# Kernel optimization log

Measured on AMD Instinct MI355X. Metric: run time of the kernel, lower is better.

Reference implementation:

```python
import jax, jax.numpy as jnp
import numpy as np

NEG_SLOPE = 0.2

def _glorot(key, shape):
    fan_in, fan_out = shape[0], shape[1]
    lim = (6.0 / (fan_in + fan_out)) ** 0.5
    return jax.random.uniform(key, shape, jnp.float32, -lim, lim)

def setup_inputs() -> dict:
    key = jax.random.key(0)
    N, E = 50000, 1000000
    node_dim, edge_dim, hidden = 64, 16, 32
    H1 = 4
    ks = jax.random.split(key, 20)
    x = jax.random.normal(ks[0], (N, node_dim), jnp.float32)
    edge_index = jax.random.randint(ks[1], (2, E), 0, N, jnp.int64)
    edge_attr = jax.random.normal(ks[2], (E, edge_dim), jnp.float32)
    d = dict(x=x, edge_index=edge_index, edge_attr=edge_attr)
    # gat1: GATv2Conv(node_dim -> hidden, heads=4, edge_dim)
    d['W1l'] = _glorot(ks[3], (node_dim, H1 * hidden)); d['b1l'] = jnp.zeros((H1 * hidden,), jnp.float32)
    d['W1r'] = _glorot(ks[4], (node_dim, H1 * hidden)); d['b1r'] = jnp.zeros((H1 * hidden,), jnp.float32)
    d['W1e'] = _glorot(ks[5], (edge_dim, H1 * hidden))
    d['att1'] = _glorot(ks[6], (H1, hidden))
    d['bias1'] = jnp.zeros((H1 * hidden,), jnp.float32)
    # gat2: GATv2Conv(4*hidden -> hidden, heads=1, edge_dim)
    d['W2l'] = _glorot(ks[7], (H1 * hidden, hidden)); d['b2l'] = jnp.zeros((hidden,), jnp.float32)
    d['W2r'] = _glorot(ks[8], (H1 * hidden, hidden)); d['b2r'] = jnp.zeros((hidden,), jnp.float32)
    d['W2e'] = _glorot(ks[9], (edge_dim, hidden))
    d['att2'] = _glorot(ks[10], (1, hidden))
    d['bias2'] = jnp.zeros((hidden,), jnp.float32)
    # edge classifier: Linear(2*hidden+edge_dim -> hidden), ReLU, Linear(hidden -> 1)
    ein = 2 * hidden + edge_dim
    d['Wc1'] = _glorot(ks[11], (ein, hidden)); d['bc1'] = jnp.zeros((hidden,), jnp.float32)
    d['Wc2'] = _glorot(ks[12], (hidden, 1)); d['bc2'] = jnp.zeros((1,), jnp.float32)
    return d

def _gatv2(x, src, dst, eattr, Wl, bl, Wr, br, We, att, bias, H, C):
    # src/dst already include self loops; eattr matches.
    N = x.shape[0]
    xl = (x @ Wl + bl).reshape(N, H, C)   # source transform
    xr = (x @ Wr + br).reshape(N, H, C)   # target transform
    ea = (eattr @ We).reshape(-1, H, C)
    m = jax.nn.leaky_relu(xl[src] + xr[dst] + ea, NEG_SLOPE)   # [E,H,C]
    alpha = jnp.einsum('ehc,hc->eh', m, att)                   # [E,H]
    amax = jax.ops.segment_max(alpha, dst, num_segments=N)
    ealpha = jnp.exp(alpha - amax[dst])
    denom = jax.ops.segment_sum(ealpha, dst, num_segments=N)
    alpha = ealpha / denom[dst]
    out = jax.ops.segment_sum(xl[src] * alpha[..., None], dst, num_segments=N)
    return out.reshape(N, H * C) + bias

def reference(x, edge_index, edge_attr, W1l, b1l, W1r, b1r, W1e, att1, bias1,
              W2l, b2l, W2r, b2r, W2e, att2, bias2, Wc1, bc1, Wc2, bc2):
    N = x.shape[0]
    src, dst = edge_index[0], edge_index[1]
    # add self loops with edge_attr fill_value='mean' (per-target mean of incoming edge attrs)
    loop_attr = jax.ops.segment_sum(edge_attr, dst, num_segments=N)
    deg = jax.ops.segment_sum(jnp.ones((dst.shape[0],), edge_attr.dtype), dst, num_segments=N)
    loop_attr = loop_attr / jnp.maximum(deg, 1.0)[:, None]
    ar = jnp.arange(N, dtype=src.dtype)
    src2 = jnp.concatenate([src, ar]); dst2 = jnp.concatenate([dst, ar])
    eattr2 = jnp.concatenate([edge_attr, loop_attr], axis=0)
    h = _gatv2(x, src2, dst2, eattr2, W1l, b1l, W1r, b1r, W1e, att1, bias1, 4, 32)
    h = jax.nn.elu(h)
    h = _gatv2(h, src2, dst2, eattr2, W2l, b2l, W2r, b2r, W2e, att2, bias2, 1, 32)
    h = jax.nn.elu(h)
    edge_emb = jnp.concatenate([h[src], h[dst]], axis=1)         # [E, 2*hidden]
    feats = jnp.concatenate([edge_emb, edge_attr], axis=1)       # [E, 2*hidden+edge_dim]
    hid = jax.nn.relu(feats @ Wc1 + bc1)
    logits = (hid @ Wc2 + bc2).squeeze(-1)                        # [E]
    return logits
```

## Files before the change

kernel.cpp:

```cpp
#include <hip/hip_runtime.h>

namespace {

constexpr int NN  = 50000;
constexpr int EE  = 1000000;
constexpr int EE2 = EE + NN;
constexpr int ND  = 64;
constexpr int F1  = 128;
constexpr int F2  = 32;
constexpr float NEG = 0.2f;

typedef unsigned short ushort_t;
typedef _Float16 half_t;
typedef _Float16 half2_t __attribute__((ext_vector_type(2)));

__device__ __forceinline__ unsigned short f2h(float f) {
  union { half_t h; unsigned short u; } c; c.h = (half_t)f; return c.u;
}
__device__ __forceinline__ float h2f(unsigned short v) {
  union { unsigned short u; half_t h; } c; c.u = v; return (float)c.h;
}
__device__ __forceinline__ half2_t u2h2(unsigned u) {
  union { unsigned u; half2_t h; } c; c.u = u; return c.h;
}
__device__ __forceinline__ unsigned pack2(float x, float y) {
  return (unsigned)f2h(x) | ((unsigned)f2h(y) << 16);
}
__device__ __forceinline__ half2_t mkh2(float x, float y) {
  half2_t r; r.x = (half_t)x; r.y = (half_t)y; return r;
}

#if __has_builtin(__builtin_amdgcn_fdot2)
#define FDOT2(a, b, c) __builtin_amdgcn_fdot2((a), (b), (c), false)
#else
#define FDOT2(a, b, c) ((float)(a).x * (float)(b).x + (float)(a).y * (float)(b).y + (c))
#endif

__global__ __launch_bounds__(256) void k_deg(const int* __restrict__ ei,
                                             int* __restrict__ deg) {
  int e = blockIdx.x * 256 + threadIdx.x;
  if (e < EE) atomicAdd(&deg[ei[EE + e]], 1);
}

__global__ __launch_bounds__(1024) void k_scan(const int* __restrict__ deg,
                                               int* __restrict__ rowstart) {
  __shared__ int sh[1024];
  int t = threadIdx.x;
  int base = t * 49;
  int end = base + 49; if (end > NN) end = NN;
  int s = 0;
  for (int i = base; i < end; ++i) s += deg[i] + 1;
  sh[t] = s;
  __syncthreads();
  for (int off = 1; off < 1024; off <<= 1) {
    int v = (t >= off) ? sh[t - off] : 0;
    __syncthreads();
    sh[t] += v;
    __syncthreads();
  }
  int run = (t == 0) ? 0 : sh[t - 1];
  for (int i = base; i < end; ++i) { rowstart[i] = run; run += deg[i] + 1; }
  if (t == 1023) rowstart[NN] = sh[1023];
}

__global__ __launch_bounds__(256) void k_fill(const int* __restrict__ ei,
                                              const float* __restrict__ edge_attr,
                                              const int* __restrict__ rowstart,
                                              int* __restrict__ cursor,
                                              int2* __restrict__ esd,
                                              ushort_t* __restrict__ eperm,
                                              int* __restrict__ loopos) {
  int i = blockIdx.x * 256 + threadIdx.x;
  if (i >= EE2) return;
  int sn, d;
  if (i < EE) { sn = ei[i]; d = ei[EE + i]; }
  else        { sn = i - EE; d = sn; }
  int pos = rowstart[d] + atomicAdd(&cursor[d], 1);
  esd[pos] = make_int2(sn, d);
  if (i < EE) {
    const float4* s4 = (const float4*)(edge_attr + (size_t)i * 16);
    float4 a = s4[0], b = s4[1], c = s4[2], e = s4[3];
    uint4 lo, hi;
    lo.x = pack2(a.x, a.y); lo.y = pack2(a.z, a.w);
    lo.z = pack2(b.x, b.y); lo.w = pack2(b.z, b.w);
    hi.x = pack2(c.x, c.y); hi.y = pack2(c.z, c.w);
    hi.z = pack2(e.x, e.y); hi.w = pack2(e.z, e.w);
    uint4* t4 = (uint4*)(eperm + (size_t)pos * 16);
    t4[0] = lo; t4[1] = hi;
  } else {
    loopos[d] = pos;
  }
}

__global__ __launch_bounds__(256) void k_loopattr(const int* __restrict__ rowstart,
                                                  const int* __restrict__ loopos,
                                                  ushort_t* __restrict__ eperm) {
  int tid = blockIdx.x * 256 + threadIdx.x;
  if (tid >= NN * 16) return;
  int n = tid >> 4, k = tid & 15;
  int s = rowstart[n], t = rowstart[n + 1];
  int lp = loopos[n];
  float acc = 0.f;
  for (int i = s; i < t; ++i) {
    if (i != lp) acc += h2f(eperm[(size_t)i * 16 + k]);
  }
  float dg = (float)(t - s - 1);
  eperm[(size_t)lp * 16 + k] = f2h(acc / fmaxf(dg, 1.f));
}

__global__ __launch_bounds__(256) void k_xprep(const float* __restrict__ x,
                                               unsigned* __restrict__ xh) {
  int tid = blockIdx.x * 256 + threadIdx.x;
  if (tid >= NN * 32) return;
  float2 v = ((const float2*)x)[tid];
  xh[tid] = pack2(v.x, v.y);
}

__global__ __launch_bounds__(256) void k_wprep(const float* __restrict__ W1l,
                                               const float* __restrict__ W1r,
                                               const float* __restrict__ W2l,
                                               const float* __restrict__ W2r,
                                               unsigned* __restrict__ W1lp,
                                               unsigned* __restrict__ W1rp,
                                               unsigned* __restrict__ W2lp,
                                               unsigned* __restrict__ W2rp) {
  int tid = blockIdx.x * 256 + threadIdx.x;
  if (tid < 32 * 128) {
    int kp = tid >> 7, j = tid & 127;
    W1lp[tid] = pack2(W1l[(2 * kp) * F1 + j], W1l[(2 * kp + 1) * F1 + j]);
    W1rp[tid] = pack2(W1r[(2 * kp) * F1 + j], W1r[(2 * kp + 1) * F1 + j]);
  }
  if (tid < 64 * 32) {
    int kp = tid >> 5, c = tid & 31;
    W2lp[tid] = pack2(W2l[(2 * kp) * F2 + c], W2l[(2 * kp + 1) * F2 + c]);
    W2rp[tid] = pack2(W2r[(2 * kp) * F2 + c], W2r[(2 * kp + 1) * F2 + c]);
  }
}

__global__ __launch_bounds__(256) void k_xform1(const unsigned* __restrict__ xh,
                                                const unsigned* __restrict__ W1lp,
                                                const unsigned* __restrict__ W1rp,
                                                const float* __restrict__ b1l,
                                                const float* __restrict__ b1r,
                                                ushort_t* __restrict__ xlh,
                                                ushort_t* __restrict__ xrh) {
  int tid = blockIdx.x * 256 + threadIdx.x;
  if (tid >= NN * 32) return;
  int n = tid >> 5, g = tid & 31;
  float4 bl = *(const float4*)(b1l + 4 * g);
  float4 br = *(const float4*)(b1r + 4 * g);
  float al0 = bl.x, al1 = bl.y, al2 = bl.z, al3 = bl.w;
  float ar0 = br.x, ar1 = br.y, ar2 = br.z, ar3 = br.w;
  const uint4* xp = (const uint4*)(xh + (size_t)n * 32);
  const uint4* wl = (const uint4*)W1lp;
  const uint4* wr = (const uint4*)W1rp;
#pragma unroll
  for (int kq = 0; kq < 8; ++kq) {
    uint4 xq = xp[kq];
    unsigned xs[4] = {xq.x, xq.y, xq.z, xq.w};
#pragma unroll
    for (int i = 0; i < 4; ++i) {
      int kp = 4 * kq + i;
      uint4 a = wl[kp * 32 + g];
      uint4 b = wr[kp * 32 + g];
      half2_t xv = u2h2(xs[i]);
      al0 = FDOT2(xv, u2h2(a.x), al0);
      al1 = FDOT2(xv, u2h2(a.y), al1);
      al2 = FDOT2(xv, u2h2(a.z), al2);
      al3 = FDOT2(xv, u2h2(a.w), al3);
      ar0 = FDOT2(xv, u2h2(b.x), ar0);
      ar1 = FDOT2(xv, u2h2(b.y), ar1);
      ar2 = FDOT2(xv, u2h2(b.z), ar2);
      ar3 = FDOT2(xv, u2h2(b.w), ar3);
    }
  }
  uint2 ol, orr;
  ol.x = pack2(al0, al1); ol.y = pack2(al2, al3);
  orr.x = pack2(ar0, ar1); orr.y = pack2(ar2, ar3);
  *(uint2*)(xlh + (size_t)n * F1 + 4 * g) = ol;
  *(uint2*)(xrh + (size_t)n * F1 + 4 * g) = orr;
}

__global__ __launch_bounds__(256, 4) void k_alpha1(const ushort_t* __restrict__ eperm,
                                                   const int2* __restrict__ esd,
                                                   const ushort_t* __restrict__ xlh,
                                                   const ushort_t* __restrict__ xrh,
                                                   const float* __restrict__ W1e,
                                                   const float* __restrict__ att1,
                                                   float* __restrict__ alpha1) {
  int lane = threadIdx.x & 63;
  int h = lane >> 4, q = lane & 15, j = h * 32 + 2 * q;
  half2_t w0p[8], w1p[8];
#pragma unroll
  for (int k = 0; k < 8; ++k) {
    w0p[k] = mkh2(W1e[(2 * k) * F1 + j],     W1e[(2 * k + 1) * F1 + j]);
    w1p[k] = mkh2(W1e[(2 * k) * F1 + j + 1], W1e[(2 * k + 1) * F1 + j + 1]);
  }
  float a0 = att1[j], a1 = att1[j + 1];
  int nw  = (gridDim.x * 256) >> 6;
  int wid = __builtin_amdgcn_readfirstlane((blockIdx.x * 256 + threadIdx.x) >> 6);
  int C = (EE2 + nw - 1) / nw;
  int start = wid * C;
  if (start >= EE2) return;
  int end = min(start + C, EE2);
  const int last = EE2 - 1;

  int2 sd0 = esd[start];
  int2 sd1 = esd[min(start + 1, last)];
  const uint4* ep0 = (const uint4*)(eperm + (size_t)start * 16);
  uint4 ca = ep0[0], cb = ep0[1];
  unsigned ul = *(const unsigned*)(xlh + (size_t)sd0.x * F1 + j);
  unsigned ur = *(const unsigned*)(xrh + (size_t)sd0.y * F1 + j);
  int dsty = sd0.y;

  for (int pos = start; pos < end; ++pos) {
    int np1 = min(pos + 1, last);
    int2 sd2 = esd[min(pos + 2, last)];
    const uint4* epn = (const uint4*)(eperm + (size_t)np1 * 16);
    uint4 na = epn[0], nb = epn[1];
    unsigned uln = *(const unsigned*)(xlh + (size_t)sd1.x * F1 + j);
    unsigned urn = (sd1.y != dsty) ? *(const unsigned*)(xrh + (size_t)sd1.y * F1 + j)
                                   : ur;
    half2_t e2[8];
    e2[0] = u2h2(ca.x); e2[1] = u2h2(ca.y); e2[2] = u2h2(ca.z); e2[3] = u2h2(ca.w);
    e2[4] = u2h2(cb.x); e2[5] = u2h2(cb.y); e2[6] = u2h2(cb.z); e2[7] = u2h2(cb.w);
    float ea0 = 0.f, ea1 = 0.f;
#pragma unroll
    for (int k = 0; k < 8; ++k) {
      ea0 = FDOT2(e2[k], w0p[k], ea0);
      ea1 = FDOT2(e2[k], w1p[k], ea1);
    }
    half2_t ul2 = u2h2(ul), ur2 = u2h2(ur);
    float m0 = (float)ul2.x + (float)ur2.x + ea0;
    float m1 = (float)ul2.y + (float)ur2.y + ea1;
    m0 = fmaxf(m0, NEG * m0);
    m1 = fmaxf(m1, NEG * m1);
    float p = a0 * m0 + a1 * m1;
#pragma unroll
    for (int m = 8; m >= 1; m >>= 1) p += __shfl_xor(p, m);
    float pe = __expf(p);
    if (q == 0) alpha1[(size_t)pos * 4 + h] = pe;
    dsty = sd1.y;
    sd1 = sd2; ca = na; cb = nb; ul = uln; ur = urn;
  }
}

__global__ __launch_bounds__(256) void k_gatB1(const int2* __restrict__ esd,
                                               const int* __restrict__ rowstart,
                                               const float* __restrict__ alpha1,
                                               const ushort_t* __restrict__ xlh,
                                               const float* __restrict__ bias1,
                                               unsigned* __restrict__ h1h) {
  int n = (blockIdx.x * 256 + threadIdx.x) >> 6;
  if (n >= NN) return;
  int lane = threadIdx.x & 63;
  int h = lane >> 4;
  int s = rowstart[n], t = rowstart[n + 1];
  const int* srcp = (const int*)esd;
  float d = 0.f, acc0 = 0.f, acc1 = 0.f;
  for (int i = s; i < t; i += 4) {
    int i1 = min(i + 1, t - 1), i2 = min(i + 2, t - 1), i3 = min(i + 3, t - 1);
    int s0 = srcp[2 * i], s1 = srcp[2 * i1], s2 = srcp[2 * i2], s3 = srcp[2 * i3];
    float W0 = alpha1[(size_t)i * 4 + h];
    float W1 = (i + 1 < t) ? alpha1[(size_t)i1 * 4 + h] : 0.f;
    float W2 = (i + 2 < t) ? alpha1[(size_t)i2 * 4 + h] : 0.f;
    float W3 = (i + 3 < t) ? alpha1[(size_t)i3 * 4 + h] : 0.f;
    unsigned g0 = *(const unsigned*)(xlh + (size_t)s0 * F1 + 2 * lane);
    unsigned g1 = *(const unsigned*)(xlh + (size_t)s1 * F1 + 2 * lane);
    unsigned g2 = *(const unsigned*)(xlh + (size_t)s2 * F1 + 2 * lane);
    unsigned g3 = *(const unsigned*)(xlh + (size_t)s3 * F1 + 2 * lane);
    d += W0 + W1 + W2 + W3;
    half2_t h0 = u2h2(g0), h1v = u2h2(g1), h2v = u2h2(g2), h3v = u2h2(g3);
    acc0 += (float)h0.x * W0 + (float)h1v.x * W1 + (float)h2v.x * W2 + (float)h3v.x * W3;
    acc1 += (float)h0.y * W0 + (float)h1v.y * W1 + (float)h2v.y * W2 + (float)h3v.y * W3;
  }
  float2 bs = *(const float2*)(bias1 + 2 * lane);
  float o0 = acc0 / d + bs.x;
  float o1 = acc1 / d + bs.y;
  o0 = o0 > 0.f ? o0 : (__expf(o0) - 1.f);
  o1 = o1 > 0.f ? o1 : (__expf(o1) - 1.f);
  h1h[(size_t)n * 64 + lane] = pack2(o0, o1);
}

__global__ __launch_bounds__(256) void k_xform2(const unsigned* __restrict__ h1h,
                                                const unsigned* __restrict__ W2lp,
                                                const unsigned* __restrict__ W2rp,
                                                const float* __restrict__ b2l,
                                                const float* __restrict__ b2r,
                                                ushort_t* __restrict__ xl2h,
                                                ushort_t* __restrict__ xr2h) {
  int tid = blockIdx.x * 256 + threadIdx.x;
  if (tid >= NN * 8) return;
  int n = tid >> 3, g = tid & 7;
  float4 bl = *(const float4*)(b2l + 4 * g);
  float4 br = *(const float4*)(b2r + 4 * g);
  float al0 = bl.x, al1 = bl.y, al2 = bl.z, al3 = bl.w;
  float ar0 = br.x, ar1 = br.y, ar2 = br.z, ar3 = br.w;
  const uint4* hp = (const uint4*)(h1h + (size_t)n * 64);
  const uint4* wl = (const uint4*)W2lp;
  const uint4* wr = (const uint4*)W2rp;
#pragma unroll 4
  for (int kq = 0; kq < 16; ++kq) {
    uint4 hq = hp[kq];
    unsigned hs[4] = {hq.x, hq.y, hq.z, hq.w};
#pragma unroll
    for (int i = 0; i < 4; ++i) {
      int kp = 4 * kq + i;
      uint4 a = wl[kp * 8 + g];
      uint4 b = wr[kp * 8 + g];
      half2_t hv = u2h2(hs[i]);
      al0 = FDOT2(hv, u2h2(a.x), al0);
      al1 = FDOT2(hv, u2h2(a.y), al1);
      al2 = FDOT2(hv, u2h2(a.z), al2);
      al3 = FDOT2(hv, u2h2(a.w), al3);
      ar0 = FDOT2(hv, u2h2(b.x), ar0);
      ar1 = FDOT2(hv, u2h2(b.y), ar1);
      ar2 = FDOT2(hv, u2h2(b.z), ar2);
      ar3 = FDOT2(hv, u2h2(b.w), ar3);
    }
  }
  uint2 ol, orr;
  ol.x = pack2(al0, al1); ol.y = pack2(al2, al3);
  orr.x = pack2(ar0, ar1); orr.y = pack2(ar2, ar3);
  *(uint2*)(xl2h + (size_t)n * F2 + 4 * g) = ol;
  *(uint2*)(xr2h + (size_t)n * F2 + 4 * g) = orr;
}

__global__ __launch_bounds__(256, 4) void k_alpha2(const ushort_t* __restrict__ eperm,
                                                   const int2* __restrict__ esd,
                                                   const ushort_t* __restrict__ xl2h,
                                                   const ushort_t* __restrict__ xr2h,
                                                   const float* __restrict__ W2e,
                                                   const float* __restrict__ att2,
                                                   float* __restrict__ alpha2) {
  int lane = threadIdx.x & 63;
  int g = lane >> 4, q = lane & 15, j = 2 * q;
  half2_t w0p[8], w1p[8];
#pragma unroll
  for (int k = 0; k < 8; ++k) {
    w0p[k] = mkh2(W2e[(2 * k) * F2 + j],     W2e[(2 * k + 1) * F2 + j]);
    w1p[k] = mkh2(W2e[(2 * k) * F2 + j + 1], W2e[(2 * k + 1) * F2 + j + 1]);
  }
  float a0 = att2[j], a1 = att2[j + 1];
  int nw  = (gridDim.x * 256) >> 6;
  int wid = __builtin_amdgcn_readfirstlane((blockIdx.x * 256 + threadIdx.x) >> 6);
  int C = (((EE2 + nw - 1) / nw) + 3) & ~3;
  int start = wid * C;
  if (start >= EE2) return;
  int end = min(start + C, EE2);
  const int last = EE2 - 1;

  int p0 = min(start + g, last);
  int2 sd0 = esd[p0];
  int2 sd1 = esd[min(start + 4 + g, last)];
  const uint4* ep0 = (const uint4*)(eperm + (size_t)p0 * 16);
  uint4 ca = ep0[0], cb = ep0[1];
  unsigned ul = *(const unsigned*)(xl2h + (size_t)sd0.x * F2 + j);
  unsigned ur = *(const unsigned*)(xr2h + (size_t)sd0.y * F2 + j);

  for (int base = start; base < end; base += 4) {
    int2 sd2 = esd[min(base + 8 + g, last)];
    const uint4* epn = (const uint4*)(eperm + (size_t)min(base + 4 + g, last) * 16);
    uint4 na = epn[0], nb = epn[1];
    unsigned uln = *(const unsigned*)(xl2h + (size_t)sd1.x * F2 + j);
    unsigned urn = *(const unsigned*)(xr2h + (size_t)sd1.y * F2 + j);
    half2_t e2[8];
    e2[0] = u2h2(ca.x); e2[1] = u2h2(ca.y); e2[2] = u2h2(ca.z); e2[3] = u2h2(ca.w);
    e2[4] = u2h2(cb.x); e2[5] = u2h2(cb.y); e2[6] = u2h2(cb.z); e2[7] = u2h2(cb.w);
    float ea = 0.f, eb = 0.f;
#pragma unroll
    for (int k = 0; k < 8; ++k) {
      ea = FDOT2(e2[k], w0p[k], ea);
      eb = FDOT2(e2[k], w1p[k], eb);
    }
    half2_t ul2 = u2h2(ul), ur2 = u2h2(ur);
    float m0 = (float)ul2.x + (float)ur2.x + ea;
    float m1 = (float)ul2.y + (float)ur2.y + eb;
    m0 = fmaxf(m0, NEG * m0);
    m1 = fmaxf(m1, NEG * m1);
    float p = a0 * m0 + a1 * m1;
#pragma unroll
    for (int m = 8; m >= 1; m >>= 1) p += __shfl_xor(p, m);
    float pe = __expf(p);
    int pos = base + g;
    if (q == 0 && pos < end) alpha2[pos] = pe;
    sd1 = sd2; ca = na; cb = nb; ul = uln; ur = urn;
  }
}

__global__ __launch_bounds__(256) void k_gatB2(const int2* __restrict__ esd,
                                               const int* __restrict__ rowstart,
                                               const float* __restrict__ alpha2,
                                               const ushort_t* __restrict__ xl2h,
                                               const float* __restrict__ bias2,
                                               float* __restrict__ h2) {
  int n = (blockIdx.x * 256 + threadIdx.x) >> 4;
  if (n >= NN) return;
  int q = threadIdx.x & 15;
  int s = rowstart[n], t = rowstart[n + 1];
  const int* srcp = (const int*)esd;
  float d = 0.f, acc0 = 0.f, acc1 = 0.f;
  for (int i = s; i < t; i += 4) {
    int i1 = min(i + 1, t - 1), i2 = min(i + 2, t - 1), i3 = min(i + 3, t - 1);
    int s0 = srcp[2 * i], s1 = srcp[2 * i1], s2 = srcp[2 * i2], s3 = srcp[2 * i3];
    float W0 = alpha2[i];
    float W1 = (i + 1 < t) ? alpha2[i1] : 0.f;
    float W2 = (i + 2 < t) ? alpha2[i2] : 0.f;
    float W3 = (i + 3 < t) ? alpha2[i3] : 0.f;
    unsigned g0 = *(const unsigned*)(xl2h + (size_t)s0 * F2 + 2 * q);
    unsigned g1 = *(const unsigned*)(xl2h + (size_t)s1 * F2 + 2 * q);
    unsigned g2 = *(const unsigned*)(xl2h + (size_t)s2 * F2 + 2 * q);
    unsigned g3 = *(const unsigned*)(xl2h + (size_t)s3 * F2 + 2 * q);
    d += W0 + W1 + W2 + W3;
    half2_t h0 = u2h2(g0), h1v = u2h2(g1), h2v = u2h2(g2), h3v = u2h2(g3);
    acc0 += (float)h0.x * W0 + (float)h1v.x * W1 + (float)h2v.x * W2 + (float)h3v.x * W3;
    acc1 += (float)h0.y * W0 + (float)h1v.y * W1 + (float)h2v.y * W2 + (float)h3v.y * W3;
  }
  float2 bs = *(const float2*)(bias2 + 2 * q);
  float o0 = acc0 / d + bs.x;
  float o1 = acc1 / d + bs.y;
  o0 = o0 > 0.f ? o0 : (__expf(o0) - 1.f);
  o1 = o1 > 0.f ? o1 : (__expf(o1) - 1.f);
  *(float2*)(h2 + (size_t)n * F2 + 2 * q) = make_float2(o0, o1);
}

__global__ __launch_bounds__(256) void k_ucls(const float* __restrict__ h2,
                                              const float* __restrict__ Wc1,
                                              float* __restrict__ us,
                                              float* __restrict__ ud) {
  int tid = blockIdx.x * 256 + threadIdx.x;
  if (tid >= NN * F2) return;
  int n = tid >> 5, c = tid & 31;
  const float* hp = h2 + (size_t)n * F2;
  float a = 0.f, b = 0.f;
#pragma unroll 8
  for (int k = 0; k < 32; ++k) {
    float hv = hp[k];
    a += hv * Wc1[k * F2 + c];
    b += hv * Wc1[(32 + k) * F2 + c];
  }
  us[tid] = a;
  ud[tid] = b;
}

__global__ __launch_bounds__(256, 4) void k_cls(const int* __restrict__ ei,
                                                const float* __restrict__ edge_attr,
                                                const float* __restrict__ us,
                                                const float* __restrict__ ud,
                                                const float* __restrict__ Wc1,
                                                const float* __restrict__ bc1,
                                                const float* __restrict__ Wc2,
                                                const float* __restrict__ bc2,
                                                float* __restrict__ out) {
  int lane = threadIdx.x & 63;
  int g = lane >> 4, q = lane & 15, j = 2 * q;
  float wk0[16], wk1[16];
#pragma unroll
  for (int k = 0; k < 16; ++k) {
    wk0[k] = Wc1[(64 + k) * F2 + j];
    wk1[k] = Wc1[(64 + k) * F2 + j + 1];
  }
  float b0 = bc1[j], b1 = bc1[j + 1], c0 = Wc2[j], c1 = Wc2[j + 1];
  float bb = bc2[0];
  int nw  = (gridDim.x * 256) >> 6;
  int wid = __builtin_amdgcn_readfirstlane((blockIdx.x * 256 + threadIdx.x) >> 6);
  int C = (((EE + nw - 1) / nw) + 3) & ~3;
  int start = wid * C;
  if (start >= EE) return;
  int end = min(start + C, EE);
  const int last = EE - 1;

  int e0c = min(start + g, last);
  int sn0 = ei[e0c], dn0 = ei[EE + e0c];
  int e1c = min(start + 4 + g, last);
  int sn1 = ei[e1c], dn1 = ei[EE + e1c];
  const float4* ep0 = (const float4*)(edge_attr + (size_t)e0c * 16);
  float4 ca0 = ep0[0], ca1 = ep0[1], ca2 = ep0[2], ca3 = ep0[3];
  float2 su = *(const float2*)(us + (size_t)sn0 * F2 + j);
  float2 du = *(const float2*)(ud + (size_t)dn0 * F2 + j);

  for (int base = start; base < end; base += 4) {
    int e2c = min(base + 8 + g, last);
    int sn2 = ei[e2c], dn2 = ei[EE + e2c];
    const float4* epn = (const float4*)(edge_attr + (size_t)min(base + 4 + g, last) * 16);
    float4 na0 = epn[0], na1 = epn[1], na2 = epn[2], na3 = epn[3];
    float2 sun = *(const float2*)(us + (size_t)sn1 * F2 + j);
    float2 dun = *(const float2*)(ud + (size_t)dn1 * F2 + j);
    float ev[16] = {ca0.x, ca0.y, ca0.z, ca0.w, ca1.x, ca1.y, ca1.z, ca1.w,
                    ca2.x, ca2.y, ca2.z, ca2.w, ca3.x, ca3.y, ca3.z, ca3.w};
    float acc0 = b0 + su.x + du.x;
    float acc1 = b1 + su.y + du.y;
#pragma unroll
    for (int k = 0; k < 16; ++k) { acc0 += ev[k] * wk0[k]; acc1 += ev[k] * wk1[k]; }
    float r = fmaxf(acc0, 0.f) * c0 + fmaxf(acc1, 0.f) * c1;
#pragma unroll
    for (int m = 8; m >= 1; m >>= 1) r += __shfl_xor(r, m);
    int e = base + g;
    if (q == 0 && e < end) out[e] = r + bb;
    sn1 = sn2; dn1 = dn2;
    ca0 = na0; ca1 = na1; ca2 = na2; ca3 = na3;
    su = sun; du = dun;
  }
}

}

extern "C" void kernel_launch(void* const* d_in, const int* in_sizes, int n_in,
                              void* d_out, int out_size, void* d_ws, size_t ws_size,
                              hipStream_t stream) {
  const float* x         = (const float*)d_in[0];
  const int*   ei        = (const int*)d_in[1];
  const float* edge_attr = (const float*)d_in[2];
  const float* W1l  = (const float*)d_in[3];
  const float* b1l  = (const float*)d_in[4];
  const float* W1r  = (const float*)d_in[5];
  const float* b1r  = (const float*)d_in[6];
  const float* W1e  = (const float*)d_in[7];
  const float* att1 = (const float*)d_in[8];
  const float* bias1= (const float*)d_in[9];
  const float* W2l  = (const float*)d_in[10];
  const float* b2l  = (const float*)d_in[11];
  const float* W2r  = (const float*)d_in[12];
  const float* b2r  = (const float*)d_in[13];
  const float* W2e  = (const float*)d_in[14];
  const float* att2 = (const float*)d_in[15];
  const float* bias2= (const float*)d_in[16];
  const float* Wc1  = (const float*)d_in[17];
  const float* bc1  = (const float*)d_in[18];
  const float* Wc2  = (const float*)d_in[19];
  const float* bc2  = (const float*)d_in[20];
  float* out = (float*)d_out;

  int*  deg      = (int*)d_ws;
  int*  cursor   = deg + NN;
  int*  loopos   = cursor + NN;
  int*  rowstart = loopos + NN;
  int2* esd      = (int2*)(rowstart + 50004 + 4);
  ushort_t* eperm = (ushort_t*)(esd + EE2);
  ushort_t* xlh  = eperm + (size_t)EE2 * 16;
  ushort_t* xrh  = xlh + (size_t)NN * F1;
  float* alpha1  = (float*)(xrh + (size_t)NN * F1);
  unsigned* h1h  = (unsigned*)(alpha1 + (size_t)EE2 * 4);
  unsigned* xh   = h1h + (size_t)NN * 64;
  unsigned* W1lp = xh + (size_t)NN * 32;
  unsigned* W1rp = W1lp + 4096;
  unsigned* W2lp = W1rp + 4096;
  unsigned* W2rp = W2lp + 2048;
  ushort_t* xl2h = xlh;
  ushort_t* xr2h = xl2h + (size_t)NN * F2;
  float* alpha2 = (float*)(xr2h + (size_t)NN * F2);
  float* h2 = alpha2 + EE2;
  float* us = h2 + (size_t)NN * F2;
  float* ud = us + (size_t)NN * F2;

  hipMemsetAsync(deg, 0, 2 * (size_t)NN * sizeof(int), stream);

  k_deg<<<(EE + 255) / 256, 256, 0, stream>>>(ei, deg);
  k_scan<<<1, 1024, 0, stream>>>(deg, rowstart);
  k_fill<<<(EE2 + 255) / 256, 256, 0, stream>>>(ei, edge_attr, rowstart, cursor,
                                                esd, eperm, loopos);
  k_loopattr<<<(NN * 16 + 255) / 256, 256, 0, stream>>>(rowstart, loopos, eperm);
  k_xprep<<<(NN * 32 + 255) / 256, 256, 0, stream>>>(x, xh);
  k_wprep<<<16, 256, 0, stream>>>(W1l, W1r, W2l, W2r, W1lp, W1rp, W2lp, W2rp);
  k_xform1<<<(NN * 32 + 255) / 256, 256, 0, stream>>>(xh, W1lp, W1rp, b1l, b1r, xlh, xrh);
  k_alpha1<<<2048, 256, 0, stream>>>(eperm, esd, xlh, xrh, W1e, att1, alpha1);
  k_gatB1<<<(NN * 64 + 255) / 256, 256, 0, stream>>>(esd, rowstart, alpha1, xlh, bias1, h1h);
  k_xform2<<<(NN * 8 + 255) / 256, 256, 0, stream>>>(h1h, W2lp, W2rp, b2l, b2r, xl2h, xr2h);
  k_alpha2<<<2048, 256, 0, stream>>>(eperm, esd, xl2h, xr2h, W2e, att2, alpha2);
  k_gatB2<<<(NN * 16 + 255) / 256, 256, 0, stream>>>(esd, rowstart, alpha2, xl2h, bias2, h2);
  k_ucls<<<(NN * F2 + 255) / 256, 256, 0, stream>>>(h2, Wc1, us, ud);
  k_cls<<<2048, 256, 0, stream>>>(ei, edge_attr, us, ud, Wc1, bc1, Wc2, bc2, out);
}
```

Baseline: 602.7 us.

## Fuse attention scoring with aggregation via per-destination running sums and atomics

The edge-score kernels now also accumulate the weighted source features and the softmax denominators while walking edges sorted by destination. Each wave flushes its partial sums with atomics whenever the destination changes. Small finalize kernels then divide, add the bias and apply ELU. This removes the per-edge alpha write and reread and the second gather pass over source features, at the cost of extra memsets, float atomics at chunk boundaries, and a nondeterministic summation order. Layer 2 also changes from strided four-group interleaving to contiguous per-group chunks.

```diff
diff --git a/kernel.cpp b/kernel.cpp
--- a/kernel.cpp
+++ b/kernel.cpp
@@ -181,13 +181,14 @@
   *(uint2*)(xrh + (size_t)n * F1 + 4 * g) = orr;
 }
 
-__global__ __launch_bounds__(256, 4) void k_alpha1(const ushort_t* __restrict__ eperm,
-                                                   const int2* __restrict__ esd,
-                                                   const ushort_t* __restrict__ xlh,
-                                                   const ushort_t* __restrict__ xrh,
-                                                   const float* __restrict__ W1e,
-                                                   const float* __restrict__ att1,
-                                                   float* __restrict__ alpha1) {
+__global__ __launch_bounds__(256, 4) void k_gat1(const ushort_t* __restrict__ eperm,
+                                                 const int2* __restrict__ esd,
+                                                 const ushort_t* __restrict__ xlh,
+                                                 const ushort_t* __restrict__ xrh,
+                                                 const float* __restrict__ W1e,
+                                                 const float* __restrict__ att1,
+                                                 float* __restrict__ h1num,
+                                                 float* __restrict__ h1den) {
   int lane = threadIdx.x & 63;
   int h = lane >> 4, q = lane & 15, j = h * 32 + 2 * q;
   half2_t w0p[8], w1p[8];
@@ -205,22 +206,23 @@
   int end = min(start + C, EE2);
   const int last = EE2 - 1;
 
-  int2 sd0 = esd[start];
+  int2 sdc = esd[start];
   int2 sd1 = esd[min(start + 1, last)];
   const uint4* ep0 = (const uint4*)(eperm + (size_t)start * 16);
   uint4 ca = ep0[0], cb = ep0[1];
-  unsigned ul = *(const unsigned*)(xlh + (size_t)sd0.x * F1 + j);
-  unsigned ur = *(const unsigned*)(xrh + (size_t)sd0.y * F1 + j);
-  int dsty = sd0.y;
+  unsigned ul = *(const unsigned*)(xlh + (size_t)sdc.x * F1 + j);
+  unsigned ur = *(const unsigned*)(xrh + (size_t)sdc.y * F1 + j);
+
+  int cur = sdc.y;
+  float num0 = 0.f, num1 = 0.f, den = 0.f;
 
   for (int pos = start; pos < end; ++pos) {
-    int np1 = min(pos + 1, last);
     int2 sd2 = esd[min(pos + 2, last)];
-    const uint4* epn = (const uint4*)(eperm + (size_t)np1 * 16);
+    const uint4* epn = (const uint4*)(eperm + (size_t)min(pos + 1, last) * 16);
     uint4 na = epn[0], nb = epn[1];
     unsigned uln = *(const unsigned*)(xlh + (size_t)sd1.x * F1 + j);
-    unsigned urn = (sd1.y != dsty) ? *(const unsigned*)(xrh + (size_t)sd1.y * F1 + j)
-                                   : ur;
+    unsigned urn = (sd1.y != sdc.y) ? *(const unsigned*)(xrh + (size_t)sd1.y * F1 + j)
+                                    : ur;
     half2_t e2[8];
     e2[0] = u2h2(ca.x); e2[1] = u2h2(ca.y); e2[2] = u2h2(ca.z); e2[3] = u2h2(ca.w);
     e2[4] = u2h2(cb.x); e2[5] = u2h2(cb.y); e2[6] = u2h2(cb.z); e2[7] = u2h2(cb.w);
@@ -239,47 +241,38 @@
 #pragma unroll
     for (int m = 8; m >= 1; m >>= 1) p += __shfl_xor(p, m);
     float pe = __expf(p);
-    if (q == 0) alpha1[(size_t)pos * 4 + h] = pe;
-    dsty = sd1.y;
-    sd1 = sd2; ca = na; cb = nb; ul = uln; ur = urn;
-  }
-}
-
-__global__ __launch_bounds__(256) void k_gatB1(const int2* __restrict__ esd,
-                                               const int* __restrict__ rowstart,
-                                               const float* __restrict__ alpha1,
-                                               const ushort_t* __restrict__ xlh,
-                                               const float* __restrict__ bias1,
-                                               unsigned* __restrict__ h1h) {
-  int n = (blockIdx.x * 256 + threadIdx.x) >> 6;
-  if (n >= NN) return;
-  int lane = threadIdx.x & 63;
-  int h = lane >> 4;
-  int s = rowstart[n], t = rowstart[n + 1];
-  const int* srcp = (const int*)esd;
-  float d = 0.f, acc0 = 0.f, acc1 = 0.f;
-  for (int i = s; i < t; i += 4) {
-    int i1 = min(i + 1, t - 1), i2 = min(i + 2, t - 1), i3 = min(i + 3, t - 1);
-    int s0 = srcp[2 * i], s1 = srcp[2 * i1], s2 = srcp[2 * i2], s3 = srcp[2 * i3];
-    float W0 = alpha1[(size_t)i * 4 + h];
-    float W1 = (i + 1 < t) ? alpha1[(size_t)i1 * 4 + h] : 0.f;
-    float W2 = (i + 2 < t) ? alpha1[(size_t)i2 * 4 + h] : 0.f;
-    float W3 = (i + 3 < t) ? alpha1[(size_t)i3 * 4 + h] : 0.f;
-    unsigned g0 = *(const unsigned*)(xlh + (size_t)s0 * F1 + 2 * lane);
-    unsigned g1 = *(const unsigned*)(xlh + (size_t)s1 * F1 + 2 * lane);
-    unsigned g2 = *(const unsigned*)(xlh + (size_t)s2 * F1 + 2 * lane);
-    unsigned g3 = *(const unsigned*)(xlh + (size_t)s3 * F1 + 2 * lane);
-    d += W0 + W1 + W2 + W3;
-    half2_t h0 = u2h2(g0), h1v = u2h2(g1), h2v = u2h2(g2), h3v = u2h2(g3);
-    acc0 += (float)h0.x * W0 + (float)h1v.x * W1 + (float)h2v.x * W2 + (float)h3v.x * W3;
-    acc1 += (float)h0.y * W0 + (float)h1v.y * W1 + (float)h2v.y * W2 + (float)h3v.y * W3;
-  }
+    if (sdc.y != cur) {
+      atomicAdd(&h1num[(size_t)cur * F1 + j], num0);
+      atomicAdd(&h1num[(size_t)cur * F1 + j + 1], num1);
+      if (q == 0) atomicAdd(&h1den[cur * 4 + h], den);
+      num0 = 0.f; num1 = 0.f; den = 0.f;
+      cur = sdc.y;
+    }
+    num0 += pe * (float)ul2.x;
+    num1 += pe * (float)ul2.y;
+    den  += pe;
+    sdc = sd1; sd1 = sd2; ca = na; cb = nb; ul = uln; ur = urn;
+  }
+  atomicAdd(&h1num[(size_t)cur * F1 + j], num0);
+  atomicAdd(&h1num[(size_t)cur * F1 + j + 1], num1);
+  if (q == 0) atomicAdd(&h1den[cur * 4 + h], den);
+}
+
+__global__ __launch_bounds__(256) void k_gatfin1(const float* __restrict__ h1num,
+                                                 const float* __restrict__ h1den,
+                                                 const float* __restrict__ bias1,
+                                                 unsigned* __restrict__ h1h) {
+  int tid = blockIdx.x * 256 + threadIdx.x;
+  if (tid >= NN * 64) return;
+  int n = tid >> 6, lane = tid & 63;
+  float2 nm = *(const float2*)(h1num + (size_t)n * F1 + 2 * lane);
+  float den = h1den[n * 4 + (lane >> 4)];
   float2 bs = *(const float2*)(bias1 + 2 * lane);
-  float o0 = acc0 / d + bs.x;
-  float o1 = acc1 / d + bs.y;
+  float o0 = nm.x / den + bs.x;
+  float o1 = nm.y / den + bs.y;
   o0 = o0 > 0.f ? o0 : (__expf(o0) - 1.f);
   o1 = o1 > 0.f ? o1 : (__expf(o1) - 1.f);
-  h1h[(size_t)n * 64 + lane] = pack2(o0, o1);
+  h1h[tid] = pack2(o0, o1);
 }
 
 __global__ __launch_bounds__(256) void k_xform2(const unsigned* __restrict__ h1h,
@@ -326,13 +319,14 @@
   *(uint2*)(xr2h + (size_t)n * F2 + 4 * g) = orr;
 }
 
-__global__ __launch_bounds__(256, 4) void k_alpha2(const ushort_t* __restrict__ eperm,
-                                                   const int2* __restrict__ esd,
-                                                   const ushort_t* __restrict__ xl2h,
-                                                   const ushort_t* __restrict__ xr2h,
-                                                   const float* __restrict__ W2e,
-                                                   const float* __restrict__ att2,
-                                                   float* __restrict__ alpha2) {
+__global__ __launch_bounds__(256, 4) void k_gat2(const ushort_t* __restrict__ eperm,
+                                                 const int2* __restrict__ esd,
+                                                 const ushort_t* __restrict__ xl2h,
+                                                 const ushort_t* __restrict__ xr2h,
+                                                 const float* __restrict__ W2e,
+                                                 const float* __restrict__ att2,
+                                                 float* __restrict__ h2num,
+                                                 float* __restrict__ h2den) {
   int lane = threadIdx.x & 63;
   int g = lane >> 4, q = lane & 15, j = 2 * q;
   half2_t w0p[8], w1p[8];
@@ -343,27 +337,32 @@
   }
   float a0 = att2[j], a1 = att2[j + 1];
   int nw  = (gridDim.x * 256) >> 6;
-  int wid = __builtin_amdgcn_readfirstlane((blockIdx.x * 256 + threadIdx.x) >> 6);
-  int C = (((EE2 + nw - 1) / nw) + 3) & ~3;
-  int start = wid * C;
+  int wid = (blockIdx.x * 256 + threadIdx.x) >> 6;
+  int ngroups = nw * 4;
+  int gid = wid * 4 + g;
+  int C = (EE2 + ngroups - 1) / ngroups;
+  int start = gid * C;
   if (start >= EE2) return;
   int end = min(start + C, EE2);
   const int last = EE2 - 1;
 
-  int p0 = min(start + g, last);
-  int2 sd0 = esd[p0];
-  int2 sd1 = esd[min(start + 4 + g, last)];
-  const uint4* ep0 = (const uint4*)(eperm + (size_t)p0 * 16);
+  int2 sdc = esd[start];
+  int2 sd1 = esd[min(start + 1, last)];
+  const uint4* ep0 = (const uint4*)(eperm + (size_t)start * 16);
   uint4 ca = ep0[0], cb = ep0[1];
-  unsigned ul = *(const unsigned*)(xl2h + (size_t)sd0.x * F2 + j);
-  unsigned ur = *(const unsigned*)(xr2h + (size_t)sd0.y * F2 + j);
-
-  for (int base = start; base < end; base += 4) {
-    int2 sd2 = esd[min(base + 8 + g, last)];
-    const uint4* epn = (const uint4*)(eperm + (size_t)min(base + 4 + g, last) * 16);
+  unsigned ul = *(const unsigned*)(xl2h + (size_t)sdc.x * F2 + j);
+  unsigned ur = *(const unsigned*)(xr2h + (size_t)sdc.y * F2 + j);
+
+  int cur = sdc.y;
+  float num0 = 0.f, num1 = 0.f, den = 0.f;
+
+  for (int pos = start; pos < end; ++pos) {
+    int2 sd2 = esd[min(pos + 2, last)];
+    const uint4* epn = (const uint4*)(eperm + (size_t)min(pos + 1, last) * 16);
     uint4 na = epn[0], nb = epn[1];
     unsigned uln = *(const unsigned*)(xl2h + (size_t)sd1.x * F2 + j);
-    unsigned urn = *(const unsigned*)(xr2h + (size_t)sd1.y * F2 + j);
+    unsigned urn = (sd1.y != sdc.y) ? *(const unsigned*)(xr2h + (size_t)sd1.y * F2 + j)
+                                    : ur;
     half2_t e2[8];
     e2[0] = u2h2(ca.x); e2[1] = u2h2(ca.y); e2[2] = u2h2(ca.z); e2[3] = u2h2(ca.w);
     e2[4] = u2h2(cb.x); e2[5] = u2h2(cb.y); e2[6] = u2h2(cb.z); e2[7] = u2h2(cb.w);
@@ -382,43 +381,35 @@
 #pragma unroll
     for (int m = 8; m >= 1; m >>= 1) p += __shfl_xor(p, m);
     float pe = __expf(p);
-    int pos = base + g;
-    if (q == 0 && pos < end) alpha2[pos] = pe;
-    sd1 = sd2; ca = na; cb = nb; ul = uln; ur = urn;
-  }
-}
-
-__global__ __launch_bounds__(256) void k_gatB2(const int2* __restrict__ esd,
-                                               const int* __restrict__ rowstart,
-                                               const float* __restrict__ alpha2,
-                                               const ushort_t* __restrict__ xl2h,
-                                               const float* __restrict__ bias2,
-                                               float* __restrict__ h2) {
-  int n = (blockIdx.x * 256 + threadIdx.x) >> 4;
-  if (n >= NN) return;
-  int q = threadIdx.x & 15;
-  int s = rowstart[n], t = rowstart[n + 1];
-  const int* srcp = (const int*)esd;
-  float d = 0.f, acc0 = 0.f, acc1 = 0.f;
-  for (int i = s; i < t; i += 4) {
-    int i1 = min(i + 1, t - 1), i2 = min(i + 2, t - 1), i3 = min(i + 3, t - 1);
-    int s0 = srcp[2 * i], s1 = srcp[2 * i1], s2 = srcp[2 * i2], s3 = srcp[2 * i3];
-    float W0 = alpha2[i];
-    float W1 = (i + 1 < t) ? alpha2[i1] : 0.f;
-    float W2 = (i + 2 < t) ? alpha2[i2] : 0.f;
-    float W3 = (i + 3 < t) ? alpha2[i3] : 0.f;
-    unsigned g0 = *(const unsigned*)(xl2h + (size_t)s0 * F2 + 2 * q);
-    unsigned g1 = *(const unsigned*)(xl2h + (size_t)s1 * F2 + 2 * q);
-    unsigned g2 = *(const unsigned*)(xl2h + (size_t)s2 * F2 + 2 * q);
-    unsigned g3 = *(const unsigned*)(xl2h + (size_t)s3 * F2 + 2 * q);
-    d += W0 + W1 + W2 + W3;
-    half2_t h0 = u2h2(g0), h1v = u2h2(g1), h2v = u2h2(g2), h3v = u2h2(g3);
-    acc0 += (float)h0.x * W0 + (float)h1v.x * W1 + (float)h2v.x * W2 + (float)h3v.x * W3;
-    acc1 += (float)h0.y * W0 + (float)h1v.y * W1 + (float)h2v.y * W2 + (float)h3v.y * W3;
-  }
+    if (sdc.y != cur) {
+      atomicAdd(&h2num[(size_t)cur * F2 + j], num0);
+      atomicAdd(&h2num[(size_t)cur * F2 + j + 1], num1);
+      if (q == 0) atomicAdd(&h2den[cur], den);
+      num0 = 0.f; num1 = 0.f; den = 0.f;
+      cur = sdc.y;
+    }
+    num0 += pe * (float)ul2.x;
+    num1 += pe * (float)ul2.y;
+    den  += pe;
+    sdc = sd1; sd1 = sd2; ca = na; cb = nb; ul = uln; ur = urn;
+  }
+  atomicAdd(&h2num[(size_t)cur * F2 + j], num0);
+  atomicAdd(&h2num[(size_t)cur * F2 + j + 1], num1);
+  if (q == 0) atomicAdd(&h2den[cur], den);
+}
+
+__global__ __launch_bounds__(256) void k_gatfin2(const float* __restrict__ h2num,
+                                                 const float* __restrict__ h2den,
+                                                 const float* __restrict__ bias2,
+                                                 float* __restrict__ h2) {
+  int tid = blockIdx.x * 256 + threadIdx.x;
+  if (tid >= NN * 16) return;
+  int n = tid >> 4, q = tid & 15;
+  float2 nm = *(const float2*)(h2num + (size_t)n * F2 + 2 * q);
+  float den = h2den[n];
   float2 bs = *(const float2*)(bias2 + 2 * q);
-  float o0 = acc0 / d + bs.x;
-  float o1 = acc1 / d + bs.y;
+  float o0 = nm.x / den + bs.x;
+  float o1 = nm.y / den + bs.y;
   o0 = o0 > 0.f ? o0 : (__expf(o0) - 1.f);
   o1 = o1 > 0.f ? o1 : (__expf(o1) - 1.f);
   *(float2*)(h2 + (size_t)n * F2 + 2 * q) = make_float2(o0, o1);
@@ -535,23 +526,25 @@
   int*  cursor   = deg + NN;
   int*  loopos   = cursor + NN;
   int*  rowstart = loopos + NN;
-  int2* esd      = (int2*)(rowstart + 50004 + 4);
+  int2* esd      = (int2*)(rowstart + 50008);
   ushort_t* eperm = (ushort_t*)(esd + EE2);
   ushort_t* xlh  = eperm + (size_t)EE2 * 16;
   ushort_t* xrh  = xlh + (size_t)NN * F1;
-  float* alpha1  = (float*)(xrh + (size_t)NN * F1);
-  unsigned* h1h  = (unsigned*)(alpha1 + (size_t)EE2 * 4);
-  unsigned* xh   = h1h + (size_t)NN * 64;
-  unsigned* W1lp = xh + (size_t)NN * 32;
+  float* h1num   = (float*)(xrh + (size_t)NN * F1);
+  float* h1den   = h1num + (size_t)NN * F1;
+  unsigned* h1h  = (unsigned*)(h1den + (size_t)NN * 4);
+  unsigned* W1lp = h1h + (size_t)NN * 64;
   unsigned* W1rp = W1lp + 4096;
   unsigned* W2lp = W1rp + 4096;
   unsigned* W2rp = W2lp + 2048;
+  unsigned* xh   = (unsigned*)h1num;
   ushort_t* xl2h = xlh;
   ushort_t* xr2h = xl2h + (size_t)NN * F2;
-  float* alpha2 = (float*)(xr2h + (size_t)NN * F2);
-  float* h2 = alpha2 + EE2;
-  float* us = h2 + (size_t)NN * F2;
-  float* ud = us + (size_t)NN * F2;
+  float* h2num   = h1num;
+  float* h2den   = h1num + (size_t)NN * F2;
+  float* h2      = h2den + NN;
+  float* us      = h2 + (size_t)NN * F2;
+  float* ud      = us + (size_t)NN * F2;
 
   hipMemsetAsync(deg, 0, 2 * (size_t)NN * sizeof(int), stream);
 
@@ -563,11 +556,13 @@
   k_xprep<<<(NN * 32 + 255) / 256, 256, 0, stream>>>(x, xh);
   k_wprep<<<16, 256, 0, stream>>>(W1l, W1r, W2l, W2r, W1lp, W1rp, W2lp, W2rp);
   k_xform1<<<(NN * 32 + 255) / 256, 256, 0, stream>>>(xh, W1lp, W1rp, b1l, b1r, xlh, xrh);
-  k_alpha1<<<2048, 256, 0, stream>>>(eperm, esd, xlh, xrh, W1e, att1, alpha1);
-  k_gatB1<<<(NN * 64 + 255) / 256, 256, 0, stream>>>(esd, rowstart, alpha1, xlh, bias1, h1h);
+  hipMemsetAsync(h1num, 0, (size_t)NN * 132 * sizeof(float), stream);
+  k_gat1<<<2048, 256, 0, stream>>>(eperm, esd, xlh, xrh, W1e, att1, h1num, h1den);
+  k_gatfin1<<<(NN * 64 + 255) / 256, 256, 0, stream>>>(h1num, h1den, bias1, h1h);
   k_xform2<<<(NN * 8 + 255) / 256, 256, 0, stream>>>(h1h, W2lp, W2rp, b2l, b2r, xl2h, xr2h);
-  k_alpha2<<<2048, 256, 0, stream>>>(eperm, esd, xl2h, xr2h, W2e, att2, alpha2);
-  k_gatB2<<<(NN * 16 + 255) / 256, 256, 0, stream>>>(esd, rowstart, alpha2, xl2h, bias2, h2);
+  hipMemsetAsync(h2num, 0, (size_t)NN * 33 * sizeof(float), stream);
+  k_gat2<<<2048, 256, 0, stream>>>(eperm, esd, xl2h, xr2h, W2e, att2, h2num, h2den);
+  k_gatfin2<<<(NN * 16 + 255) / 256, 256, 0, stream>>>(h2num, h2den, bias2, h2);
   k_ucls<<<(NN * F2 + 255) / 256, 256, 0, stream>>>(h2, Wc1, us, ud);
   k_cls<<<2048, 256, 0, stream>>>(ei, edge_attr, us, ud, Wc1, bc1, Wc2, bc2, out);
 }
```

Result: faster. 567.6 us (-5.8%).
